# Kernel tuning notes

Measured on AMD Instinct MI355X. Metric: run time of the kernel, lower is better.

The kernel has to match this reference:

```python
import jax, jax.numpy as jnp
import numpy as np

NUM_USERS = 100000
NUM_ITEMS = 50000
NUM_NODES = NUM_USERS + NUM_ITEMS
EMB = 64
NUM_EDGES = 2000000
BATCH = 16384


def setup_inputs() -> dict:
    key = jax.random.key(0)
    ks = jax.random.split(key, 9)

    def xavier(k, shape):
        fan_in, fan_out = shape[-2], shape[-1]
        lim = float(np.sqrt(6.0 / (fan_in + fan_out)))
        return jax.random.uniform(k, shape, jnp.float32, -lim, lim)

    user_table = xavier(ks[0], (NUM_USERS, EMB))
    item_table = xavier(ks[1], (NUM_ITEMS, EMB))
    # gat1: in=64, heads=4, out=64 -> W1 [64, 256]; a1 [4, 128]
    W1 = xavier(ks[2], (EMB, EMB * 4))
    a1 = xavier(ks[3], (4, 2 * EMB))
    # gat2: in=256, heads=1, out=64 -> W2 [256, 64]; a2 [1, 128]
    W2 = xavier(ks[4], (EMB * 4, EMB))
    a2 = xavier(ks[5], (1, 2 * EMB))

    edge_index = jax.random.randint(ks[6], (2, NUM_EDGES), 0, NUM_NODES, dtype=jnp.int32)
    user_ids = jax.random.randint(ks[7], (BATCH,), 0, NUM_USERS, dtype=jnp.int32)
    item_ids = jax.random.randint(ks[8], (BATCH,), 0, NUM_ITEMS, dtype=jnp.int32)
    return {
        "user_table": user_table, "item_table": item_table,
        "W1": W1, "a1": a1, "W2": W2, "a2": a2,
        "edge_index": edge_index, "user_ids": user_ids, "item_ids": item_ids,
    }


def gat_layer(x, W, a, num_heads, out_features, src, dst, concat):
    n = x.shape[0]
    h = (x @ W).reshape(n, num_heads, out_features)          # [N,H,F]
    # attention score: (cat(h_src,h_dst) * a).sum(-1) == h_src.a_l + h_dst.a_r
    a_l, a_r = a[:, :out_features], a[:, out_features:]
    e_src = jnp.einsum('nhf,hf->nh', h, a_l)                 # [N,H]
    e_dst = jnp.einsum('nhf,hf->nh', h, a_r)
    att = e_src[src] + e_dst[dst]                            # [E,H]
    att = jnp.where(att > 0, att, 0.2 * att)                 # LeakyReLU(0.2)
    att = jnp.exp(att - jnp.max(att))                        # global max, as in torch code
    att_sum = jax.ops.segment_sum(att, dst, num_segments=n)  # [N,H]
    att = att / (att_sum[dst] + 1e-8)
    msg = att[:, :, None] * h[src]                           # [E,H,F]
    out = jax.ops.segment_sum(msg, dst, num_segments=n)      # [N,H,F]
    return out.reshape(n, -1) if concat else out.mean(axis=1)


def reference(user_table, item_table, W1, a1, W2, a2, edge_index, user_ids, item_ids):
    src, dst = edge_index[0], edge_index[1]
    all_emb = jnp.concatenate([user_table, item_table], axis=0)  # [N,64]
    h = gat_layer(all_emb, W1, a1, 4, EMB, src, dst, concat=True)  # [N,256]
    h = jax.nn.elu(h)
    h = gat_layer(h, W2, a2, 1, EMB, src, dst, concat=False)       # [N,64]
    h = h + all_emb
    user_emb = h[:NUM_USERS]
    item_emb = h[NUM_USERS:]
    return jnp.sum(user_emb[user_ids] * item_emb[item_ids], axis=1)
```

## Files before the change

kernel.cpp:

```cpp
#include <hip/hip_runtime.h>
#include <cstdint>
#include <cstddef>

#define NUM_USERS 100000
#define NUM_ITEMS 50000
#define NUM_NODES 150000
#define NUM_EDGES 2000000
#define BATCH 16384
#define BSHIFT 8
#define NBUCK ((NUM_NODES + 255) >> BSHIFT)
#define PA_EDGES 8192
#define PA_BLOCKS ((NUM_EDGES + PA_EDGES - 1) / PA_EDGES)
#define NNPAD 150016
#define TBLK2 (NNPAD / 128)

typedef _Float16 hf8 __attribute__((ext_vector_type(8)));
typedef _Float16 hf4 __attribute__((ext_vector_type(4)));
typedef float fx4 __attribute__((ext_vector_type(4)));

__global__ void flag_kernel(const int* __restrict__ uid, const int* __restrict__ iid,
                            int* __restrict__ nodelist, int* __restrict__ bcnt,
                            int* __restrict__ gcnt) {
  int i = blockIdx.x * blockDim.x + threadIdx.x;
  if (i < NBUCK) bcnt[i] = 0;
  if (i < 2) gcnt[i] = 0;
  if (i < BATCH) {
    nodelist[2 * i] = uid[i];
    nodelist[2 * i + 1] = NUM_USERS + iid[i];
  }
}

__global__ __launch_bounds__(256) void bhist_kernel(const int* __restrict__ dst,
                                                    int* __restrict__ bcnt) {
  __shared__ int bh[NBUCK];
  int t = threadIdx.x;
  for (int u = t; u < NBUCK; u += 256) bh[u] = 0;
  __syncthreads();
  int base = blockIdx.x * PA_EDGES;
#pragma unroll
  for (int u = 0; u < PA_EDGES / 256; ++u) {
    int e = base + u * 256 + t;
    if (e < NUM_EDGES) atomicAdd(&bh[dst[e] >> BSHIFT], 1);
  }
  __syncthreads();
  for (int u = t; u < NBUCK; u += 256) {
    int v = bh[u];
    if (v) atomicAdd(&bcnt[u], v);
  }
}

__global__ void bscan_kernel(const int* __restrict__ bcnt, int* __restrict__ bbase,
                             int* __restrict__ bcursor, int* __restrict__ offsets) {
  __shared__ int sh[1024];
  int t = threadIdx.x;
  int v = (t < NBUCK) ? bcnt[t] : 0;
  sh[t] = v;
  __syncthreads();
  for (int off = 1; off < 1024; off <<= 1) {
    int x = (t >= off) ? sh[t - off] : 0;
    __syncthreads();
    sh[t] += x;
    __syncthreads();
  }
  if (t < NBUCK) {
    bbase[t] = sh[t] - v;
    bcursor[t] = sh[t] - v;
  }
  if (t == NBUCK - 1) {
    bbase[NBUCK] = sh[t];
    offsets[NUM_NODES] = sh[t];
  }
}

__global__ __launch_bounds__(256) void bpart_kernel(const int* __restrict__ src,
                                                    const int* __restrict__ dst,
                                                    int* __restrict__ bcursor,
                                                    int2* __restrict__ ebuf) {
  __shared__ int lcnt[NBUCK];
  __shared__ int lbase[NBUCK];
  int t = threadIdx.x;
  for (int u = t; u < NBUCK; u += 256) lcnt[u] = 0;
  __syncthreads();
  int base = blockIdx.x * PA_EDGES;
#pragma unroll
  for (int u = 0; u < PA_EDGES / 256; ++u) {
    int e = base + u * 256 + t;
    if (e < NUM_EDGES) atomicAdd(&lcnt[dst[e] >> BSHIFT], 1);
  }
  __syncthreads();
  for (int u = t; u < NBUCK; u += 256) {
    int v = lcnt[u];
    lbase[u] = v ? atomicAdd(&bcursor[u], v) : 0;
    lcnt[u] = 0;
  }
  __syncthreads();
#pragma unroll
  for (int u = 0; u < PA_EDGES / 256; ++u) {
    int e = base + u * 256 + t;
    if (e < NUM_EDGES) {
      int d = dst[e];
      int b = d >> BSHIFT;
      int p = lbase[b] + atomicAdd(&lcnt[b], 1);
      ebuf[p] = make_int2(src[e], d);
    }
  }
}

__global__ __launch_bounds__(256) void bcsr_kernel(const int2* __restrict__ ebuf,
                                                   const int* __restrict__ bbase,
                                                   int* __restrict__ offsets,
                                                   int* __restrict__ srcs) {
  __shared__ int ncnt[256];
  __shared__ int sh[256];
  __shared__ int lcur[256];
  int b = blockIdx.x;
  int t = threadIdx.x;
  int node0 = b << BSHIFT;
  int ebeg = bbase[b], eend = bbase[b + 1];
  ncnt[t] = 0;
  __syncthreads();
  for (int i = ebeg + t; i < eend; i += 256)
    atomicAdd(&ncnt[ebuf[i].y - node0], 1);
  __syncthreads();
  int v = ncnt[t];
  sh[t] = v;
  __syncthreads();
  for (int off = 1; off < 256; off <<= 1) {
    int x = (t >= off) ? sh[t - off] : 0;
    __syncthreads();
    sh[t] += x;
    __syncthreads();
  }
  int excl = ebeg + sh[t] - v;
  if (node0 + t < NUM_NODES) offsets[node0 + t] = excl;
  lcur[t] = excl;
  __syncthreads();
  for (int i = ebeg + t; i < eend; i += 256) {
    int2 ed = ebuf[i];
    int p = atomicAdd(&lcur[ed.y - node0], 1);
    srcs[p] = ed.x;
  }
}

__global__ __launch_bounds__(256) void dlist_kernel(
    const int* __restrict__ offsets, int* __restrict__ gcnt,
    int* __restrict__ Ls, int* __restrict__ Lm,
    _Float16* __restrict__ aXhi, _Float16* __restrict__ aXlo) {
  __shared__ int c0, c1, b0, b1;
  int t = threadIdx.x;
  int n = blockIdx.x * 256 + t;
  if (t == 0) { c0 = 0; c1 = 0; }
  __syncthreads();
  int cls = -1, rank = 0;
  if (n < NUM_NODES) {
    int deg = offsets[n + 1] - offsets[n];
    cls = (deg <= 16) ? 0 : 1;
    rank = atomicAdd(cls == 0 ? &c0 : &c1, 1);
  } else if (n < NNPAD) {
    float4 z = make_float4(0.f, 0.f, 0.f, 0.f);
#pragma unroll
    for (int i = 0; i < 32; ++i) {
      ((float4*)(aXhi + (size_t)n * 256))[i] = z;
      ((float4*)(aXlo + (size_t)n * 256))[i] = z;
    }
  }
  __syncthreads();
  if (t == 0) {
    b0 = atomicAdd(&gcnt[0], c0);
    b1 = atomicAdd(&gcnt[1], c1);
  }
  __syncthreads();
  if (cls == 0) Ls[b0 + rank] = n;
  else if (cls == 1) Lm[b1 + rank] = n;
}

__global__ void proj1_kernel(const float* __restrict__ W1, const float* __restrict__ a1,
                             float* __restrict__ w1a, float* __restrict__ w1b) {
  int t = threadIdx.x;
  int h = t >> 6, k = t & 63;
  float sa = 0.f, sb = 0.f;
  for (int f = 0; f < 64; ++f) {
    float w = W1[(size_t)k * 256 + h * 64 + f];
    sa += w * a1[h * 128 + f];
    sb += w * a1[h * 128 + 64 + f];
  }
  w1a[h * 64 + k] = sa;
  w1b[h * 64 + k] = sb;
}

__device__ __forceinline__ const float* row_ptr(int s, const float* __restrict__ ut,
                                                const float* __restrict__ it) {
  return (s < NUM_USERS) ? ut + (size_t)s * 64 : it + (size_t)(s - NUM_USERS) * 64;
}

__device__ __forceinline__ float lrexp(float x) {
  x = x > 0.f ? x : 0.2f * x;
  return __expf(x);
}

__device__ __forceinline__ float wnorm(float w) {
  float sum = w;
#pragma unroll
  for (int off = 32; off; off >>= 1) sum += __shfl_xor(sum, off, 64);
  return w * (1.f / (sum + 1e-8f));
}

__device__ __forceinline__ void fold4(float4& a) {
#pragma unroll
  for (int off = 16; off <= 32; off <<= 1) {
    a.x += __shfl_xor(a.x, off, 64);
    a.y += __shfl_xor(a.y, off, 64);
    a.z += __shfl_xor(a.z, off, 64);
    a.w += __shfl_xor(a.w, off, 64);
  }
}

__device__ __forceinline__ float elu(float x) {
  return x > 0.f ? x : (__expf(x) - 1.f);
}

__device__ __forceinline__ void split4(float4 o, hf4& hv, hf4& lv) {
  float a0 = o.x * 256.f, a1 = o.y * 256.f, a2 = o.z * 256.f, a3 = o.w * 256.f;
  _Float16 h0 = (_Float16)a0, h1 = (_Float16)a1;
  _Float16 h2 = (_Float16)a2, h3 = (_Float16)a3;
  hv[0] = h0; hv[1] = h1; hv[2] = h2; hv[3] = h3;
  lv[0] = (_Float16)(a0 - (float)h0);
  lv[1] = (_Float16)(a1 - (float)h1);
  lv[2] = (_Float16)(a2 - (float)h2);
  lv[3] = (_Float16)(a3 - (float)h3);
}

__device__ __forceinline__ void splitstore(_Float16* __restrict__ hi,
                                           _Float16* __restrict__ lo,
                                           size_t idx, float v) {
  v *= 256.f;
  _Float16 h = (_Float16)v;
  hi[idx] = h;
  lo[idx] = (_Float16)(v - (float)h);
}

__global__ __launch_bounds__(256) void e1g_kernel(
    const float* __restrict__ ut, const float* __restrict__ it,
    const float* __restrict__ w1a, const float* __restrict__ w1b,
    float* __restrict__ e1s, float* __restrict__ e1d) {
  int t = threadIdx.x;
  int wave = t >> 6, lane = t & 63;
  int g = lane >> 4, fl = lane & 15;
  int node = blockIdx.x * 16 + wave * 4 + g;
  bool valid = node < NUM_NODES;
  float4 xv = make_float4(0.f, 0.f, 0.f, 0.f);
  if (valid) xv = *(const float4*)(row_ptr(node, ut, it) + fl * 4);
  float ps[4], pd[4];
#pragma unroll
  for (int h = 0; h < 4; ++h) {
    float4 wa = *(const float4*)(w1a + h * 64 + fl * 4);
    float4 wb = *(const float4*)(w1b + h * 64 + fl * 4);
    ps[h] = xv.x * wa.x + xv.y * wa.y + xv.z * wa.z + xv.w * wa.w;
    pd[h] = xv.x * wb.x + xv.y * wb.y + xv.z * wb.z + xv.w * wb.w;
  }
#pragma unroll
  for (int off = 8; off; off >>= 1) {
#pragma unroll
    for (int h = 0; h < 4; ++h) {
      ps[h] += __shfl_xor(ps[h], off, 16);
      pd[h] += __shfl_xor(pd[h], off, 16);
    }
  }
  if (valid && fl == 0) {
    *(float4*)(e1s + (size_t)node * 4) = make_float4(ps[0], ps[1], ps[2], ps[3]);
    *(float4*)(e1d + (size_t)node * 4) = make_float4(pd[0], pd[1], pd[2], pd[3]);
  }
}

__global__ __launch_bounds__(256) void aggXs_kernel(
    const int* __restrict__ Ls, const int* __restrict__ gcnt,
    const int* __restrict__ offsets, const int* __restrict__ srcs,
    const float* __restrict__ e1s, const float* __restrict__ e1d,
    const float* __restrict__ ut, const float* __restrict__ it,
    _Float16* __restrict__ aXhi, _Float16* __restrict__ aXlo) {
  __shared__ int sS[4][68];
  __shared__ __align__(16) float4 sW[4][68];
  const int t = threadIdx.x;
  const int wave = t >> 6, lane = t & 63;
  const int g = lane >> 4, fl = lane & 15;
  const int cnt = gcnt[0];
  const int widx = blockIdx.x * 16 + wave * 4 + g;
  const int node = (widx < cnt) ? Ls[widx] : -1;

  int beg = 0, deg = 0;
  float4 ed = make_float4(0.f, 0.f, 0.f, 0.f);
  if (node >= 0) {
    beg = offsets[node];
    deg = offsets[node + 1] - beg;
    ed = *(const float4*)(e1d + (size_t)node * 4);
  }
  int s = 0;
  float w0 = 0.f, w1 = 0.f, w2 = 0.f, w3 = 0.f;
  if (fl < deg) {
    s = srcs[beg + fl];
    float4 ev = *(const float4*)(e1s + (size_t)s * 4);
    w0 = lrexp(ev.x + ed.x);
    w1 = lrexp(ev.y + ed.y);
    w2 = lrexp(ev.z + ed.z);
    w3 = lrexp(ev.w + ed.w);
  }
  float t0 = w0, t1 = w1, t2 = w2, t3 = w3;
#pragma unroll
  for (int off = 8; off; off >>= 1) {
    t0 += __shfl_xor(t0, off, 16);
    t1 += __shfl_xor(t1, off, 16);
    t2 += __shfl_xor(t2, off, 16);
    t3 += __shfl_xor(t3, off, 16);
  }
  w0 *= 1.f / (t0 + 1e-8f);
  w1 *= 1.f / (t1 + 1e-8f);
  w2 *= 1.f / (t2 + 1e-8f);
  w3 *= 1.f / (t3 + 1e-8f);
  sS[wave][g * 17 + fl] = s;
  sW[wave][g * 17 + fl] = make_float4(w0, w1, w2, w3);

  int md = deg;
  md = max(md, __shfl_xor(md, 16, 64));
  md = max(md, __shfl_xor(md, 32, 64));

  float4 a0 = make_float4(0.f, 0.f, 0.f, 0.f);
  float4 a1 = a0, a2 = a0, a3 = a0;
#pragma unroll 2
  for (int e = 0; e < md; ++e) {
    int se = sS[wave][g * 17 + e];
    float4 w4 = sW[wave][g * 17 + e];
    float4 xv = *(const float4*)(row_ptr(se, ut, it) + fl * 4);
    a0.x += w4.x * xv.x; a0.y += w4.x * xv.y; a0.z += w4.x * xv.z; a0.w += w4.x * xv.w;
    a1.x += w4.y * xv.x; a1.y += w4.y * xv.y; a1.z += w4.y * xv.z; a1.w += w4.y * xv.w;
    a2.x += w4.z * xv.x; a2.y += w4.z * xv.y; a2.z += w4.z * xv.z; a2.w += w4.z * xv.w;
    a3.x += w4.w * xv.x; a3.y += w4.w * xv.y; a3.z += w4.w * xv.z; a3.w += w4.w * xv.w;
  }
  if (node >= 0) {
    hf4 hv, lv;
    split4(a0, hv, lv);
    *(hf4*)(aXhi + (size_t)node * 256 + 0 * 64 + fl * 4) = hv;
    *(hf4*)(aXlo + (size_t)node * 256 + 0 * 64 + fl * 4) = lv;
    split4(a1, hv, lv);
    *(hf4*)(aXhi + (size_t)node * 256 + 1 * 64 + fl * 4) = hv;
    *(hf4*)(aXlo + (size_t)node * 256 + 1 * 64 + fl * 4) = lv;
    split4(a2, hv, lv);
    *(hf4*)(aXhi + (size_t)node * 256 + 2 * 64 + fl * 4) = hv;
    *(hf4*)(aXlo + (size_t)node * 256 + 2 * 64 + fl * 4) = lv;
    split4(a3, hv, lv);
    *(hf4*)(aXhi + (size_t)node * 256 + 3 * 64 + fl * 4) = hv;
    *(hf4*)(aXlo + (size_t)node * 256 + 3 * 64 + fl * 4) = lv;
  }
}

__global__ __launch_bounds__(256) void aggXm_kernel(
    const int* __restrict__ Lm, const int* __restrict__ gcnt,
    const int* __restrict__ offsets, const int* __restrict__ srcs,
    const float* __restrict__ e1s, const float* __restrict__ e1d,
    const float* __restrict__ ut, const float* __restrict__ it,
    _Float16* __restrict__ aXhi, _Float16* __restrict__ aXlo) {
  int wid = threadIdx.x >> 6, lane = threadIdx.x & 63;
  int idx = blockIdx.x * 4 + wid;
  if (idx >= gcnt[1]) return;
  int node = Lm[idx];
  int beg = offsets[node], end = offsets[node + 1];
  int deg = end - beg;

  float edv0 = e1d[(size_t)node * 4 + 0];
  float edv1 = e1d[(size_t)node * 4 + 1];
  float edv2 = e1d[(size_t)node * 4 + 2];
  float edv3 = e1d[(size_t)node * 4 + 3];

  if (deg <= 64) {
    int s = 0;
    float w0 = 0.f, w1 = 0.f, w2 = 0.f, w3 = 0.f;
    if (lane < deg) {
      s = srcs[beg + lane];
      float4 ev = *(const float4*)(e1s + (size_t)s * 4);
      w0 = lrexp(ev.x + edv0);
      w1 = lrexp(ev.y + edv1);
      w2 = lrexp(ev.z + edv2);
      w3 = lrexp(ev.w + edv3);
    }
    w0 = wnorm(w0);
    w1 = wnorm(w1);
    w2 = wnorm(w2);
    w3 = wnorm(w3);

    const int g = lane >> 4, fl = lane & 15;
    float4 acc0 = make_float4(0.f, 0.f, 0.f, 0.f);
    float4 acc1 = acc0, acc2 = acc0, acc3 = acc0;
#pragma unroll 4
    for (int e = 0; e < deg; e += 4) {
      int ei = e + g;
      int sg = __shfl(s, ei, 64);
      float4 xv = *(const float4*)(row_ptr(sg, ut, it) + fl * 4);
      float wg0 = __shfl(w0, ei, 64);
      acc0.x += wg0 * xv.x; acc0.y += wg0 * xv.y;
      acc0.z += wg0 * xv.z; acc0.w += wg0 * xv.w;
      float wg1 = __shfl(w1, ei, 64);
      acc1.x += wg1 * xv.x; acc1.y += wg1 * xv.y;
      acc1.z += wg1 * xv.z; acc1.w += wg1 * xv.w;
      float wg2 = __shfl(w2, ei, 64);
      acc2.x += wg2 * xv.x; acc2.y += wg2 * xv.y;
      acc2.z += wg2 * xv.z; acc2.w += wg2 * xv.w;
      float wg3 = __shfl(w3, ei, 64);
      acc3.x += wg3 * xv.x; acc3.y += wg3 * xv.y;
      acc3.z += wg3 * xv.z; acc3.w += wg3 * xv.w;
    }
    fold4(acc0); fold4(acc1); fold4(acc2); fold4(acc3);

    float4 o = (g == 0) ? acc0 : (g == 1) ? acc1 : (g == 2) ? acc2 : acc3;
    hf4 hv, lv;
    split4(o, hv, lv);
    *(hf4*)(aXhi + (size_t)node * 256 + lane * 4) = hv;
    *(hf4*)(aXlo + (size_t)node * 256 + lane * 4) = lv;
  } else {
    float s0 = 0.f, s1 = 0.f, s2 = 0.f, s3 = 0.f;
    for (int e = beg + lane; e < end; e += 64) {
      int s = srcs[e];
      float4 ev = *(const float4*)(e1s + (size_t)s * 4);
      s0 += lrexp(ev.x + edv0); s1 += lrexp(ev.y + edv1);
      s2 += lrexp(ev.z + edv2); s3 += lrexp(ev.w + edv3);
    }
#pragma unroll
    for (int off = 32; off; off >>= 1) {
      s0 += __shfl_xor(s0, off, 64);
      s1 += __shfl_xor(s1, off, 64);
      s2 += __shfl_xor(s2, off, 64);
      s3 += __shfl_xor(s3, off, 64);
    }
    float i0 = 1.f / (s0 + 1e-8f), i1 = 1.f / (s1 + 1e-8f);
    float i2 = 1.f / (s2 + 1e-8f), i3 = 1.f / (s3 + 1e-8f);
    float a0 = 0.f, a1 = 0.f, a2 = 0.f, a3 = 0.f;
    for (int e = beg; e < end; ++e) {
      int sn = srcs[e];
      float xv = row_ptr(sn, ut, it)[lane];
      float4 ev = *(const float4*)(e1s + (size_t)sn * 4);
      a0 += lrexp(ev.x + edv0) * i0 * xv;
      a1 += lrexp(ev.y + edv1) * i1 * xv;
      a2 += lrexp(ev.z + edv2) * i2 * xv;
      a3 += lrexp(ev.w + edv3) * i3 * xv;
    }
    splitstore(aXhi, aXlo, (size_t)node * 256 + 0 * 64 + lane, a0);
    splitstore(aXhi, aXlo, (size_t)node * 256 + 1 * 64 + lane, a1);
    splitstore(aXhi, aXlo, (size_t)node * 256 + 2 * 64 + lane, a2);
    splitstore(aXhi, aXlo, (size_t)node * 256 + 3 * 64 + lane, a3);
  }
}

__global__ void wprep_kernel(const float* __restrict__ W1, const float* __restrict__ W2,
                             _Float16* __restrict__ w1t_hi, _Float16* __restrict__ w1t_lo,
                             _Float16* __restrict__ w2t_hi, _Float16* __restrict__ w2t_lo) {
  int t = threadIdx.x;
  int h = t >> 6, a = t & 63;
  for (int k = 0; k < 64; ++k) {
    float w = W1[(size_t)k * 256 + h * 64 + a] * 256.f;
    _Float16 hi = (_Float16)w;
    w1t_hi[(size_t)(h * 64 + a) * 64 + k] = hi;
    w1t_lo[(size_t)(h * 64 + a) * 64 + k] = (_Float16)(w - (float)hi);

    float v = W2[(size_t)(h * 64 + k) * 64 + a] * 256.f;
    _Float16 hi2 = (_Float16)v;
    w2t_hi[(size_t)(h * 64 + a) * 64 + k] = hi2;
    w2t_lo[(size_t)(h * 64 + a) * 64 + k] = (_Float16)(v - (float)hi2);
  }
}

__device__ __forceinline__ fx4 mfma3(fx4 c, hf8 ah, hf8 al, hf8 bh, hf8 bl) {
  c = __builtin_amdgcn_mfma_f32_16x16x32_f16(ah, bh, c, 0, 0, 0);
  c = __builtin_amdgcn_mfma_f32_16x16x32_f16(al, bh, c, 0, 0, 0);
  c = __builtin_amdgcn_mfma_f32_16x16x32_f16(ah, bl, c, 0, 0, 0);
  return c;
}

__global__ __launch_bounds__(256, 2) void trans_mfma_kernel(
    const _Float16* __restrict__ aXhi, const _Float16* __restrict__ aXlo,
    const _Float16* __restrict__ w1t_hi, const _Float16* __restrict__ w1t_lo,
    const _Float16* __restrict__ w2t_hi, const _Float16* __restrict__ w2t_lo,
    const float* __restrict__ a2v,
    float* __restrict__ h2g, float* __restrict__ e2s, float* __restrict__ e2d) {
  __shared__ __align__(16) _Float16 t1hi[4][32 * 64];
  __shared__ __align__(16) _Float16 t1lo[4][32 * 64];
  const int wave = threadIdx.x >> 6;
  const int l = threadIdx.x & 63;
  const int lr = l & 15, lg = l >> 4;
  const int node0 = (blockIdx.x * 4 + wave) * 32;
  char* myhi = (char*)&t1hi[wave][0];
  char* mylo = (char*)&t1lo[wave][0];
  const float DS = 1.52587890625e-05f;

  const size_t xbase0 = (size_t)(node0 + 0 * 16 + lr) * 256 + lg * 8;
  const size_t xbase1 = (size_t)(node0 + 1 * 16 + lr) * 256 + lg * 8;

  fx4 acc2[4][2];
#pragma unroll
  for (int m = 0; m < 4; ++m)
#pragma unroll
    for (int n = 0; n < 2; ++n) acc2[m][n] = (fx4){0.f, 0.f, 0.f, 0.f};

  hf8 cxh[4], cxl[4], nxh[4], nxl[4];
#pragma unroll
  for (int ks = 0; ks < 2; ++ks) {
    cxh[ks * 2 + 0] = *(const hf8*)(aXhi + xbase0 + ks * 32);
    cxl[ks * 2 + 0] = *(const hf8*)(aXlo + xbase0 + ks * 32);
    cxh[ks * 2 + 1] = *(const hf8*)(aXhi + xbase1 + ks * 32);
    cxl[ks * 2 + 1] = *(const hf8*)(aXlo + xbase1 + ks * 32);
  }

#pragma unroll
  for (int h = 0; h < 4; ++h) {
    if (h < 3) {
#pragma unroll
      for (int ks = 0; ks < 2; ++ks) {
        nxh[ks * 2 + 0] = *(const hf8*)(aXhi + xbase0 + (h + 1) * 64 + ks * 32);
        nxl[ks * 2 + 0] = *(const hf8*)(aXlo + xbase0 + (h + 1) * 64 + ks * 32);
        nxh[ks * 2 + 1] = *(const hf8*)(aXhi + xbase1 + (h + 1) * 64 + ks * 32);
        nxl[ks * 2 + 1] = *(const hf8*)(aXlo + xbase1 + (h + 1) * 64 + ks * 32);
      }
    }

    fx4 acc1[4][2];
#pragma unroll
    for (int m = 0; m < 4; ++m)
#pragma unroll
      for (int n = 0; n < 2; ++n) acc1[m][n] = (fx4){0.f, 0.f, 0.f, 0.f};

#pragma unroll
    for (int ks = 0; ks < 2; ++ks) {
      const int ko = ks * 32 + lg * 8;
#pragma unroll
      for (int m = 0; m < 4; ++m) {
        size_t wo = (size_t)((h * 64 + m * 16 + lr) * 64 + ko);
        hf8 wah = *(const hf8*)(w1t_hi + wo);
        hf8 wal = *(const hf8*)(w1t_lo + wo);
#pragma unroll
        for (int n = 0; n < 2; ++n)
          acc1[m][n] = mfma3(acc1[m][n], wah, wal, cxh[ks * 2 + n], cxl[ks * 2 + n]);
      }
    }

#pragma unroll
    for (int m = 0; m < 4; ++m)
#pragma unroll
      for (int n = 0; n < 2; ++n) {
        hf4 hv, lv;
#pragma unroll
        for (int r = 0; r < 4; ++r) {
          float v = acc1[m][n][r] * DS;
          v = elu(v) * 256.f;
          _Float16 hi = (_Float16)v;
          hv[r] = hi;
          lv[r] = (_Float16)(v - (float)hi);
        }
        int nl = n * 16 + lr;
        int ro = (m * 32 + lg * 8) ^ ((nl & 7) << 4);
        *(hf4*)(myhi + nl * 128 + ro) = hv;
        *(hf4*)(mylo + nl * 128 + ro) = lv;
      }

#pragma unroll
    for (int ks = 0; ks < 2; ++ks) {
      const int ko = ks * 32 + lg * 8;
      hf8 tbh[2], tbl[2];
#pragma unroll
      for (int n = 0; n < 2; ++n) {
        int nl = n * 16 + lr;
        int ro = (ks * 64 + lg * 16) ^ ((nl & 7) << 4);
        tbh[n] = *(const hf8*)(myhi + nl * 128 + ro);
        tbl[n] = *(const hf8*)(mylo + nl * 128 + ro);
      }
#pragma unroll
      for (int m = 0; m < 4; ++m) {
        size_t wo = (size_t)((h * 64 + m * 16 + lr) * 64 + ko);
        hf8 wah = *(const hf8*)(w2t_hi + wo);
        hf8 wal = *(const hf8*)(w2t_lo + wo);
#pragma unroll
        for (int n = 0; n < 2; ++n)
          acc2[m][n] = mfma3(acc2[m][n], wah, wal, tbh[n], tbl[n]);
      }
    }

    if (h < 3) {
#pragma unroll
      for (int i = 0; i < 4; ++i) { cxh[i] = nxh[i]; cxl[i] = nxl[i]; }
    }
  }

  float ps[2] = {0.f, 0.f};
  float pd[2] = {0.f, 0.f};
#pragma unroll
  for (int m = 0; m < 4; ++m) {
    fx4 al = *(const fx4*)(a2v + m * 16 + lg * 4);
    fx4 ar = *(const fx4*)(a2v + 64 + m * 16 + lg * 4);
#pragma unroll
    for (int n = 0; n < 2; ++n) {
      fx4 v = acc2[m][n] * DS;
      int node = node0 + n * 16 + lr;
      if (node < NUM_NODES)
        *(fx4*)(h2g + (size_t)node * 64 + m * 16 + lg * 4) = v;
      ps[n] += v[0] * al[0] + v[1] * al[1] + v[2] * al[2] + v[3] * al[3];
      pd[n] += v[0] * ar[0] + v[1] * ar[1] + v[2] * ar[2] + v[3] * ar[3];
    }
  }
#pragma unroll
  for (int n = 0; n < 2; ++n) {
    float s = ps[n], d = pd[n];
    s += __shfl_xor(s, 16, 64);
    s += __shfl_xor(s, 32, 64);
    d += __shfl_xor(d, 16, 64);
    d += __shfl_xor(d, 32, 64);
    int node = node0 + n * 16 + lr;
    if (lg == n && node < NUM_NODES) {
      e2s[node] = s;
      e2d[node] = d;
    }
  }
}

__global__ __launch_bounds__(256) void agg2_kernel(
    const int* __restrict__ offsets, const int* __restrict__ srcs,
    const float* __restrict__ e2s, const float* __restrict__ e2d,
    const int* __restrict__ nodelist, const float* __restrict__ h2,
    const float* __restrict__ ut, const float* __restrict__ it,
    float* __restrict__ hfin) {
  int wid = threadIdx.x >> 6, lane = threadIdx.x & 63;
  int idx = blockIdx.x * 4 + wid;
  if (idx >= 2 * BATCH) return;
  int node = nodelist[idx];
  int beg = offsets[node], end = offsets[node + 1];
  int deg = end - beg;
  float edv = e2d[node];

  if (deg <= 64) {
    int s = 0;
    float w = 0.f;
    if (lane < deg) {
      s = srcs[beg + lane];
      w = lrexp(e2s[s] + edv);
    }
    w = wnorm(w);

    const int g = lane >> 4, fl = lane & 15;
    float4 acc = make_float4(0.f, 0.f, 0.f, 0.f);
#pragma unroll 4
    for (int e = 0; e < deg; e += 4) {
      int ei = e + g;
      int sg = __shfl(s, ei, 64);
      float wg = __shfl(w, ei, 64);
      float4 hv = *(const float4*)(h2 + (size_t)sg * 64 + fl * 4);
      acc.x += wg * hv.x; acc.y += wg * hv.y; acc.z += wg * hv.z; acc.w += wg * hv.w;
    }
    fold4(acc);
    if (g == 0) {
      const float* rp = (node < NUM_USERS) ? ut + (size_t)node * 64
                                           : it + (size_t)(node - NUM_USERS) * 64;
      float4 res = *(const float4*)(rp + fl * 4);
      acc.x += res.x; acc.y += res.y; acc.z += res.z; acc.w += res.w;
      *(float4*)(hfin + (size_t)node * 64 + fl * 4) = acc;
    }
  } else {
    float psum = 0.f;
    for (int e = beg + lane; e < end; e += 64) {
      int s = srcs[e];
      psum += lrexp(e2s[s] + edv);
    }
#pragma unroll
    for (int off = 32; off; off >>= 1) psum += __shfl_xor(psum, off, 64);
    float inv = 1.f / (psum + 1e-8f);
    float acc = 0.f;
    for (int e = beg; e < end; ++e) {
      int s0 = srcs[e];
      acc += lrexp(e2s[s0] + edv) * inv * h2[(size_t)s0 * 64 + lane];
    }
    float res = (node < NUM_USERS) ? ut[(size_t)node * 64 + lane]
                                   : it[(size_t)(node - NUM_USERS) * 64 + lane];
    hfin[(size_t)node * 64 + lane] = acc + res;
  }
}

__global__ __launch_bounds__(256) void final_kernel(
    const float* __restrict__ hf, const int* __restrict__ uid,
    const int* __restrict__ iid, float* __restrict__ out) {
  int wid = threadIdx.x >> 6, lane = threadIdx.x & 63;
  int idx = blockIdx.x * 4 + wid;
  if (idx >= BATCH) return;
  int u = uid[idx], v = iid[idx];
  float a = hf[(size_t)u * 64 + lane];
  float b = hf[(size_t)(NUM_USERS + v) * 64 + lane];
  float p = a * b;
#pragma unroll
  for (int off = 32; off; off >>= 1) p += __shfl_xor(p, off, 64);
  if (lane == 0) out[idx] = p;
}

extern "C" void kernel_launch(void* const* d_in, const int* in_sizes, int n_in,
                              void* d_out, int out_size, void* d_ws, size_t ws_size,
                              hipStream_t stream) {
  const float* user_table = (const float*)d_in[0];
  const float* item_table = (const float*)d_in[1];
  const float* W1 = (const float*)d_in[2];
  const float* a1 = (const float*)d_in[3];
  const float* W2 = (const float*)d_in[4];
  const float* a2 = (const float*)d_in[5];
  const int* edge_index = (const int*)d_in[6];
  const int* user_ids = (const int*)d_in[7];
  const int* item_ids = (const int*)d_in[8];
  float* out = (float*)d_out;

  const int* src = edge_index;
  const int* dst = edge_index + NUM_EDGES;

  float* ws = (float*)d_ws;
  size_t off = 0;
  auto falloc = [&](size_t n) { float* p = ws + off; off += n; return p; };
  float* h2  = falloc((size_t)NUM_NODES * 64);
  float* e1s = falloc((size_t)NUM_NODES * 4);
  float* e1d = falloc((size_t)NUM_NODES * 4);
  float* e2s = falloc(NUM_NODES);
  float* e2d = falloc(NUM_NODES);
  float* w1a = falloc(256);
  float* w1b = falloc(256);
  int* offsets  = (int*)falloc(NUM_NODES + 1);
  int* srcs     = (int*)falloc(NUM_EDGES);
  int* nodelist = (int*)falloc(2 * BATCH);
  int* bcnt     = (int*)falloc(NBUCK);
  int* bbase    = (int*)falloc(NBUCK + 1);
  int* bcursor  = (int*)falloc(NBUCK);
  int* gcnt     = (int*)falloc(2);
  int* Ls       = (int*)falloc(NNPAD);
  int* Lm       = (int*)falloc(NNPAD);
  off = (off + 3) & ~(size_t)3;
  _Float16* aggXhi = (_Float16*)(ws + off); off += (size_t)NNPAD * 128;
  _Float16* aggXlo = (_Float16*)(ws + off); off += (size_t)NNPAD * 128;

  int2* ebuf = (int2*)aggXhi;
  float* hfin = (float*)aggXhi;
  _Float16* w1t_hi = (_Float16*)falloc(4 * 64 * 64 / 2 + 16);
  _Float16* w1t_lo = (_Float16*)falloc(4 * 64 * 64 / 2 + 16);
  _Float16* w2t_hi = (_Float16*)falloc(4 * 64 * 64 / 2 + 16);
  _Float16* w2t_lo = (_Float16*)falloc(4 * 64 * 64 / 2 + 16);

  flag_kernel<<<(BATCH + 255) / 256, 256, 0, stream>>>(user_ids, item_ids,
                                                       nodelist, bcnt, gcnt);
  bhist_kernel<<<PA_BLOCKS, 256, 0, stream>>>(dst, bcnt);
  bscan_kernel<<<1, 1024, 0, stream>>>(bcnt, bbase, bcursor, offsets);
  bpart_kernel<<<PA_BLOCKS, 256, 0, stream>>>(src, dst, bcursor, ebuf);
  bcsr_kernel<<<NBUCK, 256, 0, stream>>>(ebuf, bbase, offsets, srcs);
  dlist_kernel<<<(NNPAD + 255) / 256, 256, 0, stream>>>(offsets, gcnt, Ls, Lm,
                                                        aggXhi, aggXlo);

  proj1_kernel<<<1, 256, 0, stream>>>(W1, a1, w1a, w1b);
  e1g_kernel<<<(NNPAD + 15) / 16, 256, 0, stream>>>(user_table, item_table,
                                                    w1a, w1b, e1s, e1d);

  aggXs_kernel<<<(NNPAD + 15) / 16, 256, 0, stream>>>(Ls, gcnt, offsets, srcs,
                                                      e1s, e1d, user_table,
                                                      item_table, aggXhi, aggXlo);
  aggXm_kernel<<<(NNPAD + 3) / 4, 256, 0, stream>>>(Lm, gcnt, offsets, srcs,
                                                    e1s, e1d, user_table,
                                                    item_table, aggXhi, aggXlo);
  wprep_kernel<<<1, 256, 0, stream>>>(W1, W2, w1t_hi, w1t_lo, w2t_hi, w2t_lo);
  trans_mfma_kernel<<<TBLK2, 256, 0, stream>>>(aggXhi, aggXlo,
                                               w1t_hi, w1t_lo, w2t_hi, w2t_lo,
                                               a2, h2, e2s, e2d);

  agg2_kernel<<<(2 * BATCH + 3) / 4, 256, 0, stream>>>(offsets, srcs, e2s, e2d,
                                                       nodelist, h2,
                                                       user_table, item_table, hfin);
  final_kernel<<<(BATCH + 3) / 4, 256, 0, stream>>>(hfin, user_ids, item_ids, out);
}
```

Measured before the change: 491.4 us.

## Fold degree-list and weight-prep kernels into neighbours and batch gather loads

Node classification into low- and high-degree lists moves into bcsr_kernel, and the padded-row zeroing moves into flag_kernel, which removes dlist_kernel. proj1 and wprep are merged into a single two-block prep kernel, so there are fewer launches. The small-degree aggregation now issues all 16 neighbour loads up front with a fixed trip count, and the high-degree loop issues four gathers before the FMAs, both to raise memory-level parallelism. The MFMA kernel drops its double-buffered next-head registers to cut register pressure, at the cost of less load/compute overlap.

After: 488.9 us. Within noise of the previous version (-0.5%).

```diff
diff --git a/kernel.cpp b/kernel.cpp
--- a/kernel.cpp
+++ b/kernel.cpp
@@ -20,10 +20,15 @@
 
 __global__ void flag_kernel(const int* __restrict__ uid, const int* __restrict__ iid,
                             int* __restrict__ nodelist, int* __restrict__ bcnt,
-                            int* __restrict__ gcnt) {
+                            int* __restrict__ gcnt,
+                            _Float16* __restrict__ aXhi, _Float16* __restrict__ aXlo) {
   int i = blockIdx.x * blockDim.x + threadIdx.x;
   if (i < NBUCK) bcnt[i] = 0;
   if (i < 2) gcnt[i] = 0;
+  if (i < 2048) {
+    ((float*)(aXhi + (size_t)NUM_NODES * 256))[i] = 0.f;
+    ((float*)(aXlo + (size_t)NUM_NODES * 256))[i] = 0.f;
+  }
   if (i < BATCH) {
     nodelist[2 * i] = uid[i];
     nodelist[2 * i + 1] = NUM_USERS + iid[i];
@@ -109,15 +114,20 @@
 __global__ __launch_bounds__(256) void bcsr_kernel(const int2* __restrict__ ebuf,
                                                    const int* __restrict__ bbase,
                                                    int* __restrict__ offsets,
-                                                   int* __restrict__ srcs) {
+                                                   int* __restrict__ srcs,
+                                                   int* __restrict__ gcnt,
+                                                   int* __restrict__ Ls,
+                                                   int* __restrict__ Lm) {
   __shared__ int ncnt[256];
   __shared__ int sh[256];
   __shared__ int lcur[256];
+  __shared__ int c0, c1, b0, b1;
   int b = blockIdx.x;
   int t = threadIdx.x;
   int node0 = b << BSHIFT;
   int ebeg = bbase[b], eend = bbase[b + 1];
   ncnt[t] = 0;
+  if (t == 0) { c0 = 0; c1 = 0; }
   __syncthreads();
   for (int i = ebeg + t; i < eend; i += 256)
     atomicAdd(&ncnt[ebuf[i].y - node0], 1);
@@ -134,7 +144,19 @@
   int excl = ebeg + sh[t] - v;
   if (node0 + t < NUM_NODES) offsets[node0 + t] = excl;
   lcur[t] = excl;
-  __syncthreads();
+  int cls = -1, rank = 0;
+  if (node0 + t < NUM_NODES) {
+    cls = (v <= 16) ? 0 : 1;
+    rank = atomicAdd(cls == 0 ? &c0 : &c1, 1);
+  }
+  __syncthreads();
+  if (t == 0) {
+    b0 = atomicAdd(&gcnt[0], c0);
+    b1 = atomicAdd(&gcnt[1], c1);
+  }
+  __syncthreads();
+  if (cls == 0) Ls[b0 + rank] = node0 + t;
+  else if (cls == 1) Lm[b1 + rank] = node0 + t;
   for (int i = ebeg + t; i < eend; i += 256) {
     int2 ed = ebuf[i];
     int p = atomicAdd(&lcur[ed.y - node0], 1);
@@ -142,50 +164,36 @@
   }
 }
 
-__global__ __launch_bounds__(256) void dlist_kernel(
-    const int* __restrict__ offsets, int* __restrict__ gcnt,
-    int* __restrict__ Ls, int* __restrict__ Lm,
-    _Float16* __restrict__ aXhi, _Float16* __restrict__ aXlo) {
-  __shared__ int c0, c1, b0, b1;
+__global__ void prep_kernel(const float* __restrict__ W1, const float* __restrict__ a1,
+                            const float* __restrict__ W2,
+                            float* __restrict__ w1a, float* __restrict__ w1b,
+                            _Float16* __restrict__ w1t_hi, _Float16* __restrict__ w1t_lo,
+                            _Float16* __restrict__ w2t_hi, _Float16* __restrict__ w2t_lo) {
   int t = threadIdx.x;
-  int n = blockIdx.x * 256 + t;
-  if (t == 0) { c0 = 0; c1 = 0; }
-  __syncthreads();
-  int cls = -1, rank = 0;
-  if (n < NUM_NODES) {
-    int deg = offsets[n + 1] - offsets[n];
-    cls = (deg <= 16) ? 0 : 1;
-    rank = atomicAdd(cls == 0 ? &c0 : &c1, 1);
-  } else if (n < NNPAD) {
-    float4 z = make_float4(0.f, 0.f, 0.f, 0.f);
-#pragma unroll
-    for (int i = 0; i < 32; ++i) {
-      ((float4*)(aXhi + (size_t)n * 256))[i] = z;
-      ((float4*)(aXlo + (size_t)n * 256))[i] = z;
-    }
-  }
-  __syncthreads();
-  if (t == 0) {
-    b0 = atomicAdd(&gcnt[0], c0);
-    b1 = atomicAdd(&gcnt[1], c1);
-  }
-  __syncthreads();
-  if (cls == 0) Ls[b0 + rank] = n;
-  else if (cls == 1) Lm[b1 + rank] = n;
-}
-
-__global__ void proj1_kernel(const float* __restrict__ W1, const float* __restrict__ a1,
-                             float* __restrict__ w1a, float* __restrict__ w1b) {
-  int t = threadIdx.x;
-  int h = t >> 6, k = t & 63;
-  float sa = 0.f, sb = 0.f;
-  for (int f = 0; f < 64; ++f) {
-    float w = W1[(size_t)k * 256 + h * 64 + f];
-    sa += w * a1[h * 128 + f];
-    sb += w * a1[h * 128 + 64 + f];
-  }
-  w1a[h * 64 + k] = sa;
-  w1b[h * 64 + k] = sb;
+  int h = t >> 6;
+  if (blockIdx.x == 0) {
+    int k = t & 63;
+    float sa = 0.f, sb = 0.f;
+    for (int f = 0; f < 64; ++f) {
+      float w = W1[(size_t)k * 256 + h * 64 + f];
+      sa += w * a1[h * 128 + f];
+      sb += w * a1[h * 128 + 64 + f];
+    }
+    w1a[h * 64 + k] = sa;
+    w1b[h * 64 + k] = sb;
+  } else {
+    int a = t & 63;
+    for (int k = 0; k < 64; ++k) {
+      float w = W1[(size_t)k * 256 + h * 64 + a] * 256.f;
+      _Float16 hi = (_Float16)w;
+      w1t_hi[(size_t)(h * 64 + a) * 64 + k] = hi;
+      w1t_lo[(size_t)(h * 64 + a) * 64 + k] = (_Float16)(w - (float)hi);
+      float v = W2[(size_t)(h * 64 + k) * 64 + a] * 256.f;
+      _Float16 hi2 = (_Float16)v;
+      w2t_hi[(size_t)(h * 64 + a) * 64 + k] = hi2;
+      w2t_lo[(size_t)(h * 64 + a) * 64 + k] = (_Float16)(v - (float)hi2);
+    }
+  }
 }
 
 __device__ __forceinline__ const float* row_ptr(int s, const float* __restrict__ ut,
@@ -319,17 +327,19 @@
   sS[wave][g * 17 + fl] = s;
   sW[wave][g * 17 + fl] = make_float4(w0, w1, w2, w3);
 
-  int md = deg;
-  md = max(md, __shfl_xor(md, 16, 64));
-  md = max(md, __shfl_xor(md, 32, 64));
+  float4 xr[16];
+#pragma unroll
+  for (int e = 0; e < 16; ++e) {
+    int se = sS[wave][g * 17 + e];
+    xr[e] = *(const float4*)(row_ptr(se, ut, it) + fl * 4);
+  }
 
   float4 a0 = make_float4(0.f, 0.f, 0.f, 0.f);
   float4 a1 = a0, a2 = a0, a3 = a0;
-#pragma unroll 2
-  for (int e = 0; e < md; ++e) {
-    int se = sS[wave][g * 17 + e];
+#pragma unroll
+  for (int e = 0; e < 16; ++e) {
     float4 w4 = sW[wave][g * 17 + e];
-    float4 xv = *(const float4*)(row_ptr(se, ut, it) + fl * 4);
+    float4 xv = xr[e];
     a0.x += w4.x * xv.x; a0.y += w4.x * xv.y; a0.z += w4.x * xv.z; a0.w += w4.x * xv.w;
     a1.x += w4.y * xv.x; a1.y += w4.y * xv.y; a1.z += w4.y * xv.z; a1.w += w4.y * xv.w;
     a2.x += w4.z * xv.x; a2.y += w4.z * xv.y; a2.z += w4.z * xv.z; a2.w += w4.z * xv.w;
@@ -389,23 +399,31 @@
     const int g = lane >> 4, fl = lane & 15;
     float4 acc0 = make_float4(0.f, 0.f, 0.f, 0.f);
     float4 acc1 = acc0, acc2 = acc0, acc3 = acc0;
-#pragma unroll 4
-    for (int e = 0; e < deg; e += 4) {
-      int ei = e + g;
-      int sg = __shfl(s, ei, 64);
-      float4 xv = *(const float4*)(row_ptr(sg, ut, it) + fl * 4);
-      float wg0 = __shfl(w0, ei, 64);
-      acc0.x += wg0 * xv.x; acc0.y += wg0 * xv.y;
-      acc0.z += wg0 * xv.z; acc0.w += wg0 * xv.w;
-      float wg1 = __shfl(w1, ei, 64);
-      acc1.x += wg1 * xv.x; acc1.y += wg1 * xv.y;
-      acc1.z += wg1 * xv.z; acc1.w += wg1 * xv.w;
-      float wg2 = __shfl(w2, ei, 64);
-      acc2.x += wg2 * xv.x; acc2.y += wg2 * xv.y;
-      acc2.z += wg2 * xv.z; acc2.w += wg2 * xv.w;
-      float wg3 = __shfl(w3, ei, 64);
-      acc3.x += wg3 * xv.x; acc3.y += wg3 * xv.y;
-      acc3.z += wg3 * xv.z; acc3.w += wg3 * xv.w;
+    for (int ebase = 0; ebase < deg; ebase += 16) {
+      int i0 = ebase + g, i1 = ebase + 4 + g, i2 = ebase + 8 + g, i3 = ebase + 12 + g;
+      int s0 = __shfl(s, i0, 64), s1 = __shfl(s, i1, 64);
+      int s2 = __shfl(s, i2, 64), s3 = __shfl(s, i3, 64);
+      float4 x0 = *(const float4*)(row_ptr(s0, ut, it) + fl * 4);
+      float4 x1 = *(const float4*)(row_ptr(s1, ut, it) + fl * 4);
+      float4 x2 = *(const float4*)(row_ptr(s2, ut, it) + fl * 4);
+      float4 x3 = *(const float4*)(row_ptr(s3, ut, it) + fl * 4);
+#pragma unroll
+      for (int j = 0; j < 4; ++j) {
+        int ei = ebase + j * 4 + g;
+        float4 xv = (j == 0) ? x0 : (j == 1) ? x1 : (j == 2) ? x2 : x3;
+        float wg0 = __shfl(w0, ei, 64);
+        acc0.x += wg0 * xv.x; acc0.y += wg0 * xv.y;
+        acc0.z += wg0 * xv.z; acc0.w += wg0 * xv.w;
+        float wg1 = __shfl(w1, ei, 64);
+        acc1.x += wg1 * xv.x; acc1.y += wg1 * xv.y;
+        acc1.z += wg1 * xv.z; acc1.w += wg1 * xv.w;
+        float wg2 = __shfl(w2, ei, 64);
+        acc2.x += wg2 * xv.x; acc2.y += wg2 * xv.y;
+        acc2.z += wg2 * xv.z; acc2.w += wg2 * xv.w;
+        float wg3 = __shfl(w3, ei, 64);
+        acc3.x += wg3 * xv.x; acc3.y += wg3 * xv.y;
+        acc3.z += wg3 * xv.z; acc3.w += wg3 * xv.w;
+      }
     }
     fold4(acc0); fold4(acc1); fold4(acc2); fold4(acc3);
 
@@ -445,24 +463,6 @@
     splitstore(aXhi, aXlo, (size_t)node * 256 + 1 * 64 + lane, a1);
     splitstore(aXhi, aXlo, (size_t)node * 256 + 2 * 64 + lane, a2);
     splitstore(aXhi, aXlo, (size_t)node * 256 + 3 * 64 + lane, a3);
-  }
-}
-
-__global__ void wprep_kernel(const float* __restrict__ W1, const float* __restrict__ W2,
-                             _Float16* __restrict__ w1t_hi, _Float16* __restrict__ w1t_lo,
-                             _Float16* __restrict__ w2t_hi, _Float16* __restrict__ w2t_lo) {
-  int t = threadIdx.x;
-  int h = t >> 6, a = t & 63;
-  for (int k = 0; k < 64; ++k) {
-    float w = W1[(size_t)k * 256 + h * 64 + a] * 256.f;
-    _Float16 hi = (_Float16)w;
-    w1t_hi[(size_t)(h * 64 + a) * 64 + k] = hi;
-    w1t_lo[(size_t)(h * 64 + a) * 64 + k] = (_Float16)(w - (float)hi);
-
-    float v = W2[(size_t)(h * 64 + k) * 64 + a] * 256.f;
-    _Float16 hi2 = (_Float16)v;
-    w2t_hi[(size_t)(h * 64 + a) * 64 + k] = hi2;
-    w2t_lo[(size_t)(h * 64 + a) * 64 + k] = (_Float16)(v - (float)hi2);
   }
 }
 
@@ -498,7 +498,7 @@
 #pragma unroll
     for (int n = 0; n < 2; ++n) acc2[m][n] = (fx4){0.f, 0.f, 0.f, 0.f};
 
-  hf8 cxh[4], cxl[4], nxh[4], nxl[4];
+  hf8 cxh[4], cxl[4];
 #pragma unroll
   for (int ks = 0; ks < 2; ++ks) {
     cxh[ks * 2 + 0] = *(const hf8*)(aXhi + xbase0 + ks * 32);
@@ -509,16 +509,6 @@
 
 #pragma unroll
   for (int h = 0; h < 4; ++h) {
-    if (h < 3) {
-#pragma unroll
-      for (int ks = 0; ks < 2; ++ks) {
-        nxh[ks * 2 + 0] = *(const hf8*)(aXhi + xbase0 + (h + 1) * 64 + ks * 32);
-        nxl[ks * 2 + 0] = *(const hf8*)(aXlo + xbase0 + (h + 1) * 64 + ks * 32);
-        nxh[ks * 2 + 1] = *(const hf8*)(aXhi + xbase1 + (h + 1) * 64 + ks * 32);
-        nxl[ks * 2 + 1] = *(const hf8*)(aXlo + xbase1 + (h + 1) * 64 + ks * 32);
-      }
-    }
-
     fx4 acc1[4][2];
 #pragma unroll
     for (int m = 0; m < 4; ++m)
@@ -536,6 +526,16 @@
 #pragma unroll
         for (int n = 0; n < 2; ++n)
           acc1[m][n] = mfma3(acc1[m][n], wah, wal, cxh[ks * 2 + n], cxl[ks * 2 + n]);
+      }
+    }
+
+    if (h < 3) {
+#pragma unroll
+      for (int ks = 0; ks < 2; ++ks) {
+        cxh[ks * 2 + 0] = *(const hf8*)(aXhi + xbase0 + (h + 1) * 64 + ks * 32);
+        cxl[ks * 2 + 0] = *(const hf8*)(aXlo + xbase0 + (h + 1) * 64 + ks * 32);
+        cxh[ks * 2 + 1] = *(const hf8*)(aXhi + xbase1 + (h + 1) * 64 + ks * 32);
+        cxl[ks * 2 + 1] = *(const hf8*)(aXlo + xbase1 + (h + 1) * 64 + ks * 32);
       }
     }
 
@@ -578,11 +578,6 @@
         for (int n = 0; n < 2; ++n)
           acc2[m][n] = mfma3(acc2[m][n], wah, wal, tbh[n], tbl[n]);
       }
-    }
-
-    if (h < 3) {
-#pragma unroll
-      for (int i = 0; i < 4; ++i) { cxh[i] = nxh[i]; cxl[i] = nxl[i]; }
     }
   }
 
@@ -741,15 +736,16 @@
   _Float16* w2t_lo = (_Float16*)falloc(4 * 64 * 64 / 2 + 16);
 
   flag_kernel<<<(BATCH + 255) / 256, 256, 0, stream>>>(user_ids, item_ids,
-                                                       nodelist, bcnt, gcnt);
+                                                       nodelist, bcnt, gcnt,
+                                                       aggXhi, aggXlo);
   bhist_kernel<<<PA_BLOCKS, 256, 0, stream>>>(dst, bcnt);
   bscan_kernel<<<1, 1024, 0, stream>>>(bcnt, bbase, bcursor, offsets);
   bpart_kernel<<<PA_BLOCKS, 256, 0, stream>>>(src, dst, bcursor, ebuf);
-  bcsr_kernel<<<NBUCK, 256, 0, stream>>>(ebuf, bbase, offsets, srcs);
-  dlist_kernel<<<(NNPAD + 255) / 256, 256, 0, stream>>>(offsets, gcnt, Ls, Lm,
-                                                        aggXhi, aggXlo);
-
-  proj1_kernel<<<1, 256, 0, stream>>>(W1, a1, w1a, w1b);
+  bcsr_kernel<<<NBUCK, 256, 0, stream>>>(ebuf, bbase, offsets, srcs,
+                                         gcnt, Ls, Lm);
+
+  prep_kernel<<<2, 256, 0, stream>>>(W1, a1, W2, w1a, w1b,
+                                     w1t_hi, w1t_lo, w2t_hi, w2t_lo);
   e1g_kernel<<<(NNPAD + 15) / 16, 256, 0, stream>>>(user_table, item_table,
                                                     w1a, w1b, e1s, e1d);
 
@@ -759,7 +755,6 @@
   aggXm_kernel<<<(NNPAD + 3) / 4, 256, 0, stream>>>(Lm, gcnt, offsets, srcs,
                                                     e1s, e1d, user_table,
                                                     item_table, aggXhi, aggXlo);
-  wprep_kernel<<<1, 256, 0, stream>>>(W1, W2, w1t_hi, w1t_lo, w2t_hi, w2t_lo);
   trans_mfma_kernel<<<TBLK2, 256, 0, stream>>>(aggXhi, aggXlo,
                                                w1t_hi, w1t_lo, w2t_hi, w2t_lo,
                                                a2, h2, e2s, e2d);
```
